# Performance work log

Measured on AMD Instinct MI355X. Metric: run time of the kernel, lower is better.

Reference implementation:

```python
import jax, jax.numpy as jnp
import numpy as np

N = 50000      # nodes
E = 600000     # edges
D = 128        # embedding_dim
H = 256        # GENConv MLP hidden = 2*D (expansion=2, num_layers=2)
L = 2          # n_layers
EPS_MSG = 1e-7
EPS_NORM = 1e-5


def setup_inputs() -> dict:
    key = jax.random.key(0)
    ks = jax.random.split(key, 16)
    s = 0.05
    inp = {}
    inp["x"] = jax.random.normal(ks[0], (N, 1), jnp.float32)
    inp["edge_index"] = jax.random.randint(ks[1], (2, E), 0, N)
    inp["edge_attr"] = jax.random.normal(ks[2], (E, 1), jnp.float32)
    # encoders
    inp["Wn"] = jax.random.normal(ks[3], (1, D), jnp.float32) * s
    inp["bn_b"] = jnp.zeros((D,), jnp.float32)
    inp["We"] = jax.random.normal(ks[4], (1, D), jnp.float32) * s
    inp["be"] = jnp.zeros((D,), jnp.float32)
    # per-layer BatchNorm affine
    inp["bn_gamma"] = jnp.ones((L, D), jnp.float32)
    inp["bn_beta"] = jnp.zeros((L, D), jnp.float32)
    # per-layer GENConv params: learnable temperature t, MLP [D->H->D] with LayerNorm
    inp["t"] = jnp.ones((L,), jnp.float32)
    inp["W1"] = jax.random.normal(ks[5], (L, D, H), jnp.float32) * s
    inp["b1"] = jnp.zeros((L, H), jnp.float32)
    inp["ln_g"] = jnp.ones((L, H), jnp.float32)
    inp["ln_b"] = jnp.zeros((L, H), jnp.float32)
    inp["W2"] = jax.random.normal(ks[6], (L, H, D), jnp.float32) * s
    inp["b2"] = jnp.zeros((L, D), jnp.float32)
    return inp


def _segment_softmax(logits, seg, num):
    # per-channel softmax over edges grouped by destination node
    m = jax.ops.segment_max(logits, seg, num_segments=num)
    m = jnp.where(jnp.isfinite(m), m, 0.0)  # empty segments
    ex = jnp.exp(logits - m[seg])
    den = jax.ops.segment_sum(ex, seg, num_segments=num)
    return ex / (den[seg] + 1e-16)


def reference(x, edge_index, edge_attr, Wn, bn_b, We, be,
              bn_gamma, bn_beta, t, W1, b1, ln_g, ln_b, W2, b2):
    src, dst = edge_index[0], edge_index[1]
    h = x @ Wn + bn_b                 # [N, D] node encoder
    e = edge_attr @ We + be           # [E, D] edge encoder
    for l in range(L):
        # DeepGCNLayer 'res+': h_in -> BN -> ReLU -> conv -> + h_in
        mu = h.mean(axis=0)
        var = h.var(axis=0)
        hn = (h - mu) / jnp.sqrt(var + EPS_NORM) * bn_gamma[l] + bn_beta[l]
        hn = jax.nn.relu(hn)
        # GENConv: msg = relu(x_j + e) + eps; softmax-aggr with temperature t
        msg = jax.nn.relu(hn[src] + e) + EPS_MSG          # [E, D]
        alpha = _segment_softmax(msg * t[l], dst, N)      # [E, D]
        agg = jax.ops.segment_sum(msg * alpha, dst, num_segments=N)  # [N, D]
        out = agg + hn                                    # add root
        # GENConv MLP: Linear -> LayerNorm -> ReLU -> Linear
        z = out @ W1[l] + b1[l]
        zm = z.mean(axis=-1, keepdims=True)
        zv = z.var(axis=-1, keepdims=True)
        z = (z - zm) / jnp.sqrt(zv + EPS_NORM) * ln_g[l] + ln_b[l]
        z = jax.nn.relu(z)
        z = z @ W2[l] + b2[l]
        h = h + z                                         # res+ residual
    # DotProductPredictor over the same edge list
    return (h[src] * h[dst]).sum(axis=-1)                 # [E]
```

## Files before the change

kernel.cpp:

```cpp
#include <hip/hip_runtime.h>
#include <hip/hip_bf16.h>
#include <math.h>

#define NN 50000
#define NE 600000
#define MPAD 50048
#define NS32 (MPAD / 32)
#define DIM 128
#define HID 256
#define NB 49
#define HIST_BLOCKS ((NE + 255) / 256)
#define CAST_BLOCKS ((4 * DIM * HID) / 256)
#define EPS_MSG 1e-7f
#define EPS_NORM 1e-5f

typedef __attribute__((ext_vector_type(8))) short short8v;
typedef __attribute__((ext_vector_type(8))) unsigned short ushort8v;
typedef __attribute__((ext_vector_type(4))) float f32x4;

__device__ inline ushort f2bf(float f) {
    union { float f; unsigned u; } v; v.f = f;
    unsigned r = v.u + 0x7FFF + ((v.u >> 16) & 1);
    return (ushort)(r >> 16);
}
__device__ inline float bf2f(ushort u) {
    union { unsigned u; float f; } v; v.u = (unsigned)u << 16; return v.f;
}

__global__ __launch_bounds__(256) void k_setup(const float* __restrict__ x,
                                               const int* __restrict__ dst,
                                               const float* __restrict__ W1,
                                               const float* __restrict__ W2,
                                               float* __restrict__ xs,
                                               int* __restrict__ deg,
                                               ushort* __restrict__ W1t,
                                               ushort* __restrict__ W2t) {
    int b = blockIdx.x;
    if (b < 64) {
        int lane = threadIdx.x & 63;
        float s = 0.f, q = 0.f;
        for (int i = b * 256 + threadIdx.x; i < NN; i += 64 * 256) {
            float v = x[i];
            s += v; q += v * v;
        }
        #pragma unroll
        for (int off = 32; off >= 1; off >>= 1) {
            s += __shfl_xor(s, off, 64);
            q += __shfl_xor(q, off, 64);
        }
        if (lane == 0) { atomicAdd(&xs[0], s); atomicAdd(&xs[1], q); }
    } else if (b < 64 + HIST_BLOCKS) {
        int i = (b - 64) * 256 + threadIdx.x;
        if (i < NE) atomicAdd(&deg[dst[i]], 1);
    } else {
        const int chunk = DIM * HID;
        int i = (b - 64 - HIST_BLOCKS) * 256 + threadIdx.x;
        int w = i / chunk;
        int j = i - w * chunk;
        if (w < 2) {
            int r = j / HID, c = j - r * HID;
            W1t[(size_t)w * chunk + (size_t)c * DIM + r] = f2bf(W1[(size_t)w * chunk + j]);
        } else {
            int l = w - 2;
            int r = j / DIM, c = j - r * DIM;
            W2t[(size_t)l * chunk + (size_t)c * HID + r] = f2bf(W2[(size_t)l * chunk + j]);
        }
    }
}

__global__ void k_hn0(const float* __restrict__ x, const float* __restrict__ xs,
                      const float* __restrict__ Wn, const float* __restrict__ bnb,
                      const float* __restrict__ gamma, const float* __restrict__ beta,
                      ushort* __restrict__ hn, int total4) {
    int i = blockIdx.x * blockDim.x + threadIdx.x;
    if (i >= total4) return;
    int d4 = (i & 31) * 4;
    int n = i >> 5;
    float mx = xs[0] * (1.f / NN);
    float vx = xs[1] * (1.f / NN) - mx * mx;
    float xv = x[n];
    float4 w = *(const float4*)(Wn + d4);
    float4 b = *(const float4*)(bnb + d4);
    float4 g = *(const float4*)(gamma + d4);
    float4 bt = *(const float4*)(beta + d4);
    ushort4 o;
    {
        float mu = fmaf(mx, w.x, b.x), sc = rsqrtf(vx * w.x * w.x + EPS_NORM) * g.x;
        o.x = f2bf(fmaxf(fmaf(fmaf(xv, w.x, b.x) - mu, sc, bt.x), 0.f));
    }
    {
        float mu = fmaf(mx, w.y, b.y), sc = rsqrtf(vx * w.y * w.y + EPS_NORM) * g.y;
        o.y = f2bf(fmaxf(fmaf(fmaf(xv, w.y, b.y) - mu, sc, bt.y), 0.f));
    }
    {
        float mu = fmaf(mx, w.z, b.z), sc = rsqrtf(vx * w.z * w.z + EPS_NORM) * g.z;
        o.z = f2bf(fmaxf(fmaf(fmaf(xv, w.z, b.z) - mu, sc, bt.z), 0.f));
    }
    {
        float mu = fmaf(mx, w.w, b.w), sc = rsqrtf(vx * w.w * w.w + EPS_NORM) * g.w;
        o.w = f2bf(fmaxf(fmaf(fmaf(xv, w.w, b.w) - mu, sc, bt.w), 0.f));
    }
    *(ushort4*)(hn + (size_t)n * DIM + d4) = o;
}

__global__ __launch_bounds__(256) void k_scanA(const int* __restrict__ deg,
                                               int* __restrict__ partials, int n) {
    __shared__ int ws[4];
    int b = blockIdx.x;
    int t = threadIdx.x;
    int s = 0;
    #pragma unroll
    for (int i = 0; i < 4; ++i) {
        int idx = b * 1024 + t + i * 256;
        s += (idx < n) ? deg[idx] : 0;
    }
    #pragma unroll
    for (int off = 32; off >= 1; off >>= 1) s += __shfl_xor(s, off, 64);
    if ((t & 63) == 0) ws[t >> 6] = s;
    __syncthreads();
    if (t == 0) partials[b] = ws[0] + ws[1] + ws[2] + ws[3];
}

__global__ __launch_bounds__(64) void k_scanB(const int* __restrict__ partials,
                                              int* __restrict__ base,
                                              int* __restrict__ row_off) {
    int t = threadIdx.x;
    int v = (t < NB) ? partials[t] : 0;
    int x = v;
    #pragma unroll
    for (int off = 1; off < 64; off <<= 1) {
        int y = __shfl_up(x, off, 64);
        if (t >= off) x += y;
    }
    if (t < NB) base[t] = x - v;
    if (t == 0) row_off[NN] = NE;
}

__global__ __launch_bounds__(1024) void k_scanC(const int* __restrict__ deg,
                                                const int* __restrict__ base,
                                                int* __restrict__ row_off,
                                                int* __restrict__ cursor, int n) {
    __shared__ int wsum[16];
    int i = blockIdx.x * 1024 + threadIdx.x;
    int lane = threadIdx.x & 63;
    int wid = threadIdx.x >> 6;
    int v = (i < n) ? deg[i] : 0;
    int x = v;
    #pragma unroll
    for (int off = 1; off < 64; off <<= 1) {
        int y = __shfl_up(x, off, 64);
        if (lane >= off) x += y;
    }
    if (lane == 63) wsum[wid] = x;
    __syncthreads();
    if (wid == 0 && lane < 16) {
        int w = wsum[lane];
        #pragma unroll
        for (int off = 1; off < 16; off <<= 1) {
            int y = __shfl_up(w, off, 64);
            if (lane >= off) w += y;
        }
        wsum[lane] = w;
    }
    __syncthreads();
    int prev = (wid == 0) ? 0 : wsum[wid - 1];
    int excl = base[blockIdx.x] + prev + (x - v);
    if (i < n) { row_off[i] = excl; cursor[i] = excl; }
}

__global__ void k_scatter(const int* __restrict__ src, const int* __restrict__ dst,
                          const float* __restrict__ eattr, int* __restrict__ cursor,
                          unsigned long long* __restrict__ erec, int E) {
    int i = blockIdx.x * blockDim.x + threadIdx.x;
    if (i >= E) return;
    int d = dst[i];
    int pos = atomicAdd(&cursor[d], 1);
    unsigned long long r = (unsigned long long)(unsigned)src[i]
                         | ((unsigned long long)(unsigned)i << 16)
                         | ((unsigned long long)f2bf(eattr[i]) << 36);
    erec[pos] = r;
}

__global__ __launch_bounds__(256) void k_bn_stats(const float* __restrict__ h,
                                                  float* __restrict__ stats) {
    __shared__ float red[2][128];
    int d = threadIdx.x & 127;
    int rsub = threadIdx.x >> 7;
    float s = 0.f, q = 0.f;
    for (int r = blockIdx.x * 2 + rsub; r < NN; r += gridDim.x * 2) {
        float v = h[(size_t)r * DIM + d];
        s += v; q += v * v;
    }
    if (rsub == 0) { red[0][d] = s; red[1][d] = q; }
    __syncthreads();
    if (rsub == 1) {
        atomicAdd(&stats[d], s + red[0][d]);
        atomicAdd(&stats[DIM + d], q + red[1][d]);
    }
}

__global__ void k_bn_relu(const float* __restrict__ h, const float* __restrict__ stats,
                          const float* __restrict__ gamma, const float* __restrict__ beta,
                          ushort* __restrict__ hn, int total4) {
    int i = blockIdx.x * blockDim.x + threadIdx.x;
    if (i >= total4) return;
    int d4 = (i & 31) * 4;
    int n = i >> 5;
    float4 v = *(const float4*)(h + (size_t)n * DIM + d4);
    float4 s = *(const float4*)(stats + d4);
    float4 q = *(const float4*)(stats + DIM + d4);
    float4 g = *(const float4*)(gamma + d4);
    float4 bt = *(const float4*)(beta + d4);
    ushort4 o;
    {
        float mu = s.x * (1.f / NN), var = q.x * (1.f / NN) - mu * mu;
        float sc = rsqrtf(var + EPS_NORM) * g.x;
        o.x = f2bf(fmaxf(fmaf(v.x - mu, sc, bt.x), 0.f));
    }
    {
        float mu = s.y * (1.f / NN), var = q.y * (1.f / NN) - mu * mu;
        float sc = rsqrtf(var + EPS_NORM) * g.y;
        o.y = f2bf(fmaxf(fmaf(v.y - mu, sc, bt.y), 0.f));
    }
    {
        float mu = s.z * (1.f / NN), var = q.z * (1.f / NN) - mu * mu;
        float sc = rsqrtf(var + EPS_NORM) * g.z;
        o.z = f2bf(fmaxf(fmaf(v.z - mu, sc, bt.z), 0.f));
    }
    {
        float mu = s.w * (1.f / NN), var = q.w * (1.f / NN) - mu * mu;
        float sc = rsqrtf(var + EPS_NORM) * g.w;
        o.w = f2bf(fmaxf(fmaf(v.w - mu, sc, bt.w), 0.f));
    }
    *(ushort4*)(hn + (size_t)n * DIM + d4) = o;
}

__global__ __launch_bounds__(256) void k_agg(const ushort* __restrict__ hn,
                                             const unsigned long long* __restrict__ erec,
                                             const int* __restrict__ row_off,
                                             const float* __restrict__ We,
                                             const float* __restrict__ be,
                                             const float* __restrict__ t_all, int l,
                                             ushort* __restrict__ ob, int N) {
    int n = blockIdx.x * 4 + (threadIdx.x >> 6);
    if (n >= N) return;
    int lane = threadIdx.x & 63;
    int d0 = lane * 2;
    float2 we = *(const float2*)(We + d0);
    float2 bd = *(const float2*)(be + d0);
    float t = t_all[l];
    int p0 = row_off[n], p1 = row_off[n + 1];
    int deg = p1 - p0;

    int mp = p0 + lane;
    unsigned long long r_l = (mp < p1) ? erec[mp] : 0ull;

    float den0 = 0.f, num0 = 0.f, den1 = 0.f, num1 = 0.f;
    int kmax = deg < 64 ? deg : 64;
    int k = 0;
    for (; k + 8 <= kmax; k += 8) {
        int ss[8]; float ee[8]; uint hv[8];
        #pragma unroll
        for (int u = 0; u < 8; ++u) {
            unsigned long long r = __shfl(r_l, k + u, 64);
            ss[u] = (int)(r & 0xFFFF);
            ee[u] = bf2f((ushort)(r >> 36));
        }
        #pragma unroll
        for (int u = 0; u < 8; ++u)
            hv[u] = *(const uint*)(hn + (size_t)ss[u] * DIM + d0);
        #pragma unroll
        for (int u = 0; u < 8; ++u) {
            float m0 = fmaxf(bf2f((ushort)hv[u]) + fmaf(ee[u], we.x, bd.x), 0.f) + EPS_MSG;
            float m1 = fmaxf(bf2f((ushort)(hv[u] >> 16)) + fmaf(ee[u], we.y, bd.y), 0.f) + EPS_MSG;
            float x0 = __expf(m0 * t), x1 = __expf(m1 * t);
            den0 += x0; num0 += m0 * x0; den1 += x1; num1 += m1 * x1;
        }
    }
    for (; k < kmax; ++k) {
        unsigned long long r = __shfl(r_l, k, 64);
        int s = (int)(r & 0xFFFF);
        float ea = bf2f((ushort)(r >> 36));
        uint hv = *(const uint*)(hn + (size_t)s * DIM + d0);
        float m0 = fmaxf(bf2f((ushort)hv) + fmaf(ea, we.x, bd.x), 0.f) + EPS_MSG;
        float m1 = fmaxf(bf2f((ushort)(hv >> 16)) + fmaf(ea, we.y, bd.y), 0.f) + EPS_MSG;
        float x0 = __expf(m0 * t), x1 = __expf(m1 * t);
        den0 += x0; num0 += m0 * x0; den1 += x1; num1 += m1 * x1;
    }
    for (int p = p0 + 64; p < p1; ++p) {
        unsigned long long r = erec[p];
        int s = (int)(r & 0xFFFF);
        float ea = bf2f((ushort)(r >> 36));
        uint hv = *(const uint*)(hn + (size_t)s * DIM + d0);
        float m0 = fmaxf(bf2f((ushort)hv) + fmaf(ea, we.x, bd.x), 0.f) + EPS_MSG;
        float m1 = fmaxf(bf2f((ushort)(hv >> 16)) + fmaf(ea, we.y, bd.y), 0.f) + EPS_MSG;
        float x0 = __expf(m0 * t), x1 = __expf(m1 * t);
        den0 += x0; num0 += m0 * x0; den1 += x1; num1 += m1 * x1;
    }
    uint hr = *(const uint*)(hn + (size_t)n * DIM + d0);
    float a0 = (deg > 0) ? num0 / (den0 + 1e-16f) : 0.f;
    float a1 = (deg > 0) ? num1 / (den1 + 1e-16f) : 0.f;
    uint o = (uint)f2bf(a0 + bf2f((ushort)hr)) |
             ((uint)f2bf(a1 + bf2f((ushort)(hr >> 16))) << 16);
    *(uint*)(ob + (size_t)n * DIM + d0) = o;
}

template <int FIRST>
__global__ __launch_bounds__(256, 1) void k_mlpw(const ushort* __restrict__ A,
                                                 const ushort* __restrict__ B1t,
                                                 const float* __restrict__ b1,
                                                 const float* __restrict__ g,
                                                 const float* __restrict__ bv,
                                                 const ushort* __restrict__ B2t,
                                                 const float* __restrict__ b2,
                                                 const float* __restrict__ x,
                                                 const float* __restrict__ Wn,
                                                 const float* __restrict__ bnb,
                                                 const float* __restrict__ Cin,
                                                 float* __restrict__ Cout,
                                                 ushort* __restrict__ hb,
                                                 ushort* Z) {
    constexpr int LW1 = 130;
    constexpr int LW2 = 258;
    __shared__ ushort W1s[256 * LW1];
    __shared__ ushort W2s[128 * LW2];
    const int tid = threadIdx.x;
    const int lane = tid & 63;
    const int wid = tid >> 6;
    const int l15 = lane & 15;
    const int lq = lane >> 4;

    #pragma unroll
    for (int i = 0; i < 16; ++i) {
        int e = (tid + i * 256) * 8;
        int r = e >> 7, c = e & 127;
        *(short8v*)(W1s + r * LW1 + c) = *(const short8v*)(B1t + r * 128 + c);
    }
    #pragma unroll
    for (int i = 0; i < 16; ++i) {
        int e = (tid + i * 256) * 8;
        int r = e >> 8, c = e & 255;
        *(short8v*)(W2s + r * LW2 + c) = *(const short8v*)(B2t + r * 256 + c);
    }
    float bb[16], gg[16], lb[16];
    #pragma unroll
    for (int nf = 0; nf < 16; ++nf) {
        int col = nf * 16 + l15;
        bb[nf] = b1[col]; gg[nf] = g[col]; lb[nf] = bv[col];
    }
    float b2v[8], wnc[8], bnc[8];
    #pragma unroll
    for (int nf = 0; nf < 8; ++nf) {
        int col = nf * 16 + l15;
        b2v[nf] = b2[col];
        wnc[nf] = FIRST ? Wn[col] : 0.f;
        bnc[nf] = FIRST ? bnb[col] : 0.f;
    }
    __syncthreads();

    for (int s = blockIdx.x * 4 + wid; s < NS32; s += 1024) {
        const int row0 = s * 32;
        short8v afr[4][2];
        #pragma unroll
        for (int ks = 0; ks < 4; ++ks)
            #pragma unroll
            for (int mi = 0; mi < 2; ++mi)
                afr[ks][mi] = *(const short8v*)(A + (size_t)(row0 + mi * 16 + l15) * DIM +
                                                ks * 32 + lq * 8);
        f32x4 acc[16][2] = {};
        #pragma unroll
        for (int ks = 0; ks < 4; ++ks) {
            int kk = ks * 32 + lq * 8;
            #pragma unroll
            for (int nf = 0; nf < 16; ++nf) {
                short8v bfr = *(const short8v*)(W1s + (nf * 16 + l15) * LW1 + kk);
                #pragma unroll
                for (int mi = 0; mi < 2; ++mi)
                    acc[nf][mi] = __builtin_amdgcn_mfma_f32_16x16x32_bf16(
                        afr[ks][mi], bfr, acc[nf][mi], 0, 0, 0);
            }
        }
        #pragma unroll
        for (int mi = 0; mi < 2; ++mi) {
            #pragma unroll
            for (int j = 0; j < 4; ++j) {
                float sum = 0.f, sq = 0.f;
                #pragma unroll
                for (int nf = 0; nf < 16; ++nf) {
                    float v = acc[nf][mi][j] + bb[nf];
                    acc[nf][mi][j] = v;
                    sum += v; sq += v * v;
                }
                #pragma unroll
                for (int off = 1; off <= 8; off <<= 1) {
                    sum += __shfl_xor(sum, off, 64);
                    sq += __shfl_xor(sq, off, 64);
                }
                float mu = sum * (1.f / HID);
                float var = sq * (1.f / HID) - mu * mu;
                float rs = rsqrtf(var + EPS_NORM);
                size_t rbase = (size_t)(row0 + mi * 16 + lq * 4 + j) * HID;
                #pragma unroll
                for (int nf = 0; nf < 16; ++nf) {
                    float v = fmaxf(fmaf((acc[nf][mi][j] - mu) * rs, gg[nf], lb[nf]), 0.f);
                    Z[rbase + nf * 16 + l15] = f2bf(v);
                }
            }
        }
        asm volatile("s_waitcnt vmcnt(0)" ::: "memory");
        short8v af2[2][8];
        #pragma unroll
        for (int mi = 0; mi < 2; ++mi)
            #pragma unroll
            for (int ks = 0; ks < 8; ++ks)
                af2[mi][ks] = *(const short8v*)(Z + (size_t)(row0 + mi * 16 + l15) * HID +
                                                ks * 32 + lq * 8);
        f32x4 acc2[8][2] = {};
        #pragma unroll
        for (int ks = 0; ks < 8; ++ks) {
            int kk = ks * 32 + lq * 8;
            #pragma unroll
            for (int nf = 0; nf < 8; ++nf) {
                short8v bf2 = *(const short8v*)(W2s + (nf * 16 + l15) * LW2 + kk);
                #pragma unroll
                for (int mi = 0; mi < 2; ++mi)
                    acc2[nf][mi] = __builtin_amdgcn_mfma_f32_16x16x32_bf16(
                        af2[mi][ks], bf2, acc2[nf][mi], 0, 0, 0);
            }
        }
        #pragma unroll
        for (int mi = 0; mi < 2; ++mi) {
            #pragma unroll
            for (int j = 0; j < 4; ++j) {
                int gr = row0 + mi * 16 + lq * 4 + j;
                float xb = 0.f;
                if (FIRST) xb = (gr < NN) ? x[gr] : 0.f;
                size_t rbase = (size_t)gr * DIM;
                #pragma unroll
                for (int nf = 0; nf < 8; ++nf) {
                    int col = nf * 16 + l15;
                    float base = FIRST ? fmaf(xb, wnc[nf], bnc[nf]) : Cin[rbase + col];
                    float v = acc2[nf][mi][j] + b2v[nf] + base;
                    if (FIRST) Cout[rbase + col] = v;
                    else hb[rbase + col] = f2bf(v);
                }
            }
        }
    }
}

__global__ __launch_bounds__(256) void k_dot(const ushort* __restrict__ hb,
                                             const unsigned long long* __restrict__ erec,
                                             const int* __restrict__ row_off,
                                             float* __restrict__ out, int N) {
    int n = blockIdx.x * 4 + (threadIdx.x >> 6);
    if (n >= N) return;
    int lane = threadIdx.x & 63;
    int sub = lane >> 4;
    int l16 = lane & 15;
    float hd[8];
    {
        ushort8v hv = *(const ushort8v*)(hb + (size_t)n * DIM + l16 * 8);
        #pragma unroll
        for (int j = 0; j < 8; ++j) hd[j] = bf2f(hv[j]);
    }
    int p0 = row_off[n], p1 = row_off[n + 1];
    int deg = p1 - p0;
    int mp = p0 + lane;
    unsigned long long r_l = (mp < p1) ? erec[mp] : 0ull;
    int kmax = deg < 64 ? deg : 64;
    for (int k = 0; k < kmax; k += 4) {
        int idx = k + sub;
        bool ok = idx < kmax;
        unsigned long long r = __shfl(r_l, idx, 64);
        int s = (int)(r & 0xFFFF);
        int e = (int)((r >> 16) & 0xFFFFF);
        ushort8v av = *(const ushort8v*)(hb + (size_t)(ok ? s : n) * DIM + l16 * 8);
        float p = 0.f;
        #pragma unroll
        for (int j = 0; j < 8; ++j) p = fmaf(bf2f(av[j]), hd[j], p);
        p += __shfl_xor(p, 1, 16);
        p += __shfl_xor(p, 2, 16);
        p += __shfl_xor(p, 4, 16);
        p += __shfl_xor(p, 8, 16);
        if (ok && l16 == 0) out[e] = p;
    }
    for (int pb = p0 + 64; pb < p1; pb += 4) {
        int pe = pb + sub;
        bool ok = pe < p1;
        int s = n, e = 0;
        if (ok) {
            unsigned long long r = erec[pe];
            s = (int)(r & 0xFFFF);
            e = (int)((r >> 16) & 0xFFFFF);
        }
        ushort8v av = *(const ushort8v*)(hb + (size_t)s * DIM + l16 * 8);
        float p = 0.f;
        #pragma unroll
        for (int j = 0; j < 8; ++j) p = fmaf(bf2f(av[j]), hd[j], p);
        p += __shfl_xor(p, 1, 16);
        p += __shfl_xor(p, 2, 16);
        p += __shfl_xor(p, 4, 16);
        p += __shfl_xor(p, 8, 16);
        if (ok && l16 == 0) out[e] = p;
    }
}

extern "C" void kernel_launch(void* const* d_in, const int* in_sizes, int n_in,
                              void* d_out, int out_size, void* d_ws, size_t ws_size,
                              hipStream_t stream) {
    const float* x        = (const float*)d_in[0];
    const int*   ei       = (const int*)d_in[1];
    const float* eattr    = (const float*)d_in[2];
    const float* Wn       = (const float*)d_in[3];
    const float* bnb      = (const float*)d_in[4];
    const float* We       = (const float*)d_in[5];
    const float* be       = (const float*)d_in[6];
    const float* bn_gamma = (const float*)d_in[7];
    const float* bn_beta  = (const float*)d_in[8];
    const float* t_all    = (const float*)d_in[9];
    const float* W1       = (const float*)d_in[10];
    const float* b1       = (const float*)d_in[11];
    const float* ln_g     = (const float*)d_in[12];
    const float* ln_b     = (const float*)d_in[13];
    const float* W2       = (const float*)d_in[14];
    const float* b2       = (const float*)d_in[15];
    float* out = (float*)d_out;

    const int N = NN, E = NE, D = DIM, H = HID;
    const int* src = ei;
    const int* dst = ei + E;

    char* ws = (char*)d_ws;
    auto alloc = [&](size_t bytes) {
        char* p = ws;
        ws += (bytes + 255) & ~(size_t)255;
        return p;
    };
    float*  h       = (float*)alloc((size_t)MPAD * D * 4);
    ushort* z       = (ushort*)alloc((size_t)MPAD * H * 2);
    ushort* ob      = (ushort*)alloc((size_t)MPAD * D * 2);
    ushort* hn      = (ushort*)alloc((size_t)MPAD * D * 2);
    ushort* hb      = (ushort*)alloc((size_t)MPAD * D * 2);
    ushort* W1t     = (ushort*)alloc((size_t)2 * D * H * 2);
    ushort* W2t     = (ushort*)alloc((size_t)2 * D * H * 2);
    unsigned long long* erec = (unsigned long long*)alloc((size_t)E * 8);
    int*    row_off = (int*)alloc((size_t)(N + 1) * 4);
    int*    cursor  = (int*)alloc((size_t)N * 4);
    int*    deg     = (int*)alloc((size_t)N * 4);
    int*    partials= (int*)alloc((size_t)64 * 4);
    int*    pbase   = (int*)alloc((size_t)64 * 4);
    float*  stats   = (float*)alloc((size_t)2 * D * 4);
    float*  xs      = (float*)alloc((size_t)2 * 4);

    hipMemsetAsync(deg, 0, (size_t)N * 4, stream);
    hipMemsetAsync(stats, 0, 1024 + 8, stream);

    k_setup<<<64 + HIST_BLOCKS + CAST_BLOCKS, 256, 0, stream>>>(x, dst, W1, W2,
                                                                xs, deg, W1t, W2t);
    k_scanA<<<NB, 256, 0, stream>>>(deg, partials, N);
    k_scanB<<<1, 64, 0, stream>>>(partials, pbase, row_off);
    k_scanC<<<NB, 1024, 0, stream>>>(deg, pbase, row_off, cursor, N);
    k_scatter<<<(E + 255) / 256, 256, 0, stream>>>(src, dst, eattr, cursor, erec, E);
    k_hn0<<<(N * 32 + 255) / 256, 256, 0, stream>>>(x, xs, Wn, bnb, bn_gamma, bn_beta,
                                                    hn, N * 32);

    k_agg<<<(N + 3) / 4, 256, 0, stream>>>(hn, erec, row_off, We, be, t_all, 0, ob, N);
    k_mlpw<1><<<256, 256, 0, stream>>>(ob, W1t, b1, ln_g, ln_b, W2t, b2,
                                       x, Wn, bnb, h, h, hb, z);
    k_bn_stats<<<256, 256, 0, stream>>>(h, stats);
    k_bn_relu<<<(N * 32 + 255) / 256, 256, 0, stream>>>(h, stats, bn_gamma + D, bn_beta + D,
                                                        hn, N * 32);

    k_agg<<<(N + 3) / 4, 256, 0, stream>>>(hn, erec, row_off, We, be, t_all, 1, ob, N);
    k_mlpw<0><<<256, 256, 0, stream>>>(ob, W1t + (size_t)D * H, b1 + H,
                                       ln_g + H, ln_b + H, W2t + (size_t)D * H, b2 + D,
                                       x, Wn, bnb, h, h, hb, z);

    k_dot<<<(N + 3) / 4, 256, 0, stream>>>(hb, erec, row_off, out, N);
}
```

Measured before the change: 396.4 us.

## Fuse BN statistics into MLP kernel, keep Z in LDS, store h as bf16

The first-layer MLP kernel now accumulates per-channel BatchNorm sums and squared sums in registers and adds them atomically, so the separate k_bn_stats pass is removed. The hidden activation Z stays in a per-wave XOR-swizzled LDS tile instead of a round trip through global memory. The fp32 h buffer is replaced by bf16 hb. Blocks drop to 3 waves, each handling 16-row tiles, to fit the extra LDS. Keeping the residual stream in bf16 lowers precision, and the MLP blocks have fewer waves to hide latency.

```diff
diff --git a/kernel.cpp b/kernel.cpp
--- a/kernel.cpp
+++ b/kernel.cpp
@@ -5,7 +5,7 @@
 #define NN 50000
 #define NE 600000
 #define MPAD 50048
-#define NS32 (MPAD / 32)
+#define NHS (MPAD / 16)
 #define DIM 128
 #define HID 256
 #define NB 49
@@ -13,6 +13,8 @@
 #define CAST_BLOCKS ((4 * DIM * HID) / 256)
 #define EPS_MSG 1e-7f
 #define EPS_NORM 1e-5f
+#define MLPW_WAVES 3
+#define MLPW_THREADS (MLPW_WAVES * 64)
 
 typedef __attribute__((ext_vector_type(8))) short short8v;
 typedef __attribute__((ext_vector_type(8))) unsigned short ushort8v;
@@ -181,32 +183,14 @@
     erec[pos] = r;
 }
 
-__global__ __launch_bounds__(256) void k_bn_stats(const float* __restrict__ h,
-                                                  float* __restrict__ stats) {
-    __shared__ float red[2][128];
-    int d = threadIdx.x & 127;
-    int rsub = threadIdx.x >> 7;
-    float s = 0.f, q = 0.f;
-    for (int r = blockIdx.x * 2 + rsub; r < NN; r += gridDim.x * 2) {
-        float v = h[(size_t)r * DIM + d];
-        s += v; q += v * v;
-    }
-    if (rsub == 0) { red[0][d] = s; red[1][d] = q; }
-    __syncthreads();
-    if (rsub == 1) {
-        atomicAdd(&stats[d], s + red[0][d]);
-        atomicAdd(&stats[DIM + d], q + red[1][d]);
-    }
-}
-
-__global__ void k_bn_relu(const float* __restrict__ h, const float* __restrict__ stats,
+__global__ void k_bn_relu(const ushort* __restrict__ hb, const float* __restrict__ stats,
                           const float* __restrict__ gamma, const float* __restrict__ beta,
                           ushort* __restrict__ hn, int total4) {
     int i = blockIdx.x * blockDim.x + threadIdx.x;
     if (i >= total4) return;
     int d4 = (i & 31) * 4;
     int n = i >> 5;
-    float4 v = *(const float4*)(h + (size_t)n * DIM + d4);
+    ushort4 hv = *(const ushort4*)(hb + (size_t)n * DIM + d4);
     float4 s = *(const float4*)(stats + d4);
     float4 q = *(const float4*)(stats + DIM + d4);
     float4 g = *(const float4*)(gamma + d4);
@@ -215,22 +199,22 @@
     {
         float mu = s.x * (1.f / NN), var = q.x * (1.f / NN) - mu * mu;
         float sc = rsqrtf(var + EPS_NORM) * g.x;
-        o.x = f2bf(fmaxf(fmaf(v.x - mu, sc, bt.x), 0.f));
+        o.x = f2bf(fmaxf(fmaf(bf2f(hv.x) - mu, sc, bt.x), 0.f));
     }
     {
         float mu = s.y * (1.f / NN), var = q.y * (1.f / NN) - mu * mu;
         float sc = rsqrtf(var + EPS_NORM) * g.y;
-        o.y = f2bf(fmaxf(fmaf(v.y - mu, sc, bt.y), 0.f));
+        o.y = f2bf(fmaxf(fmaf(bf2f(hv.y) - mu, sc, bt.y), 0.f));
     }
     {
         float mu = s.z * (1.f / NN), var = q.z * (1.f / NN) - mu * mu;
         float sc = rsqrtf(var + EPS_NORM) * g.z;
-        o.z = f2bf(fmaxf(fmaf(v.z - mu, sc, bt.z), 0.f));
+        o.z = f2bf(fmaxf(fmaf(bf2f(hv.z) - mu, sc, bt.z), 0.f));
     }
     {
         float mu = s.w * (1.f / NN), var = q.w * (1.f / NN) - mu * mu;
         float sc = rsqrtf(var + EPS_NORM) * g.w;
-        o.w = f2bf(fmaxf(fmaf(v.w - mu, sc, bt.w), 0.f));
+        o.w = f2bf(fmaxf(fmaf(bf2f(hv.w) - mu, sc, bt.w), 0.f));
     }
     *(ushort4*)(hn + (size_t)n * DIM + d4) = o;
 }
@@ -306,41 +290,42 @@
 }
 
 template <int FIRST>
-__global__ __launch_bounds__(256, 1) void k_mlpw(const ushort* __restrict__ A,
-                                                 const ushort* __restrict__ B1t,
-                                                 const float* __restrict__ b1,
-                                                 const float* __restrict__ g,
-                                                 const float* __restrict__ bv,
-                                                 const ushort* __restrict__ B2t,
-                                                 const float* __restrict__ b2,
-                                                 const float* __restrict__ x,
-                                                 const float* __restrict__ Wn,
-                                                 const float* __restrict__ bnb,
-                                                 const float* __restrict__ Cin,
-                                                 float* __restrict__ Cout,
-                                                 ushort* __restrict__ hb,
-                                                 ushort* Z) {
-    constexpr int LW1 = 130;
-    constexpr int LW2 = 258;
-    __shared__ ushort W1s[256 * LW1];
-    __shared__ ushort W2s[128 * LW2];
+__global__ __launch_bounds__(MLPW_THREADS, 1) void k_mlpw(const ushort* __restrict__ A,
+                                                          const ushort* __restrict__ B1t,
+                                                          const float* __restrict__ b1,
+                                                          const float* __restrict__ g,
+                                                          const float* __restrict__ bv,
+                                                          const ushort* __restrict__ B2t,
+                                                          const float* __restrict__ b2,
+                                                          const float* __restrict__ x,
+                                                          const float* __restrict__ Wn,
+                                                          const float* __restrict__ bnb,
+                                                          const ushort* hbin,
+                                                          ushort* hbout,
+                                                          float* __restrict__ stats) {
+    __shared__ ushort W1s[256 * 128];
+    __shared__ ushort W2s[128 * 256];
+    __shared__ ushort Zs[MLPW_WAVES][16 * 256];
     const int tid = threadIdx.x;
     const int lane = tid & 63;
     const int wid = tid >> 6;
     const int l15 = lane & 15;
     const int lq = lane >> 4;
-
-    #pragma unroll
-    for (int i = 0; i < 16; ++i) {
-        int e = (tid + i * 256) * 8;
-        int r = e >> 7, c = e & 127;
-        *(short8v*)(W1s + r * LW1 + c) = *(const short8v*)(B1t + r * 128 + c);
-    }
-    #pragma unroll
-    for (int i = 0; i < 16; ++i) {
-        int e = (tid + i * 256) * 8;
-        int r = e >> 8, c = e & 255;
-        *(short8v*)(W2s + r * LW2 + c) = *(const short8v*)(B2t + r * 256 + c);
+    char* const w1b = (char*)W1s;
+    char* const w2b = (char*)W2s;
+    char* const zb = (char*)Zs[wid];
+
+    for (int c = tid; c < 4096; c += MLPW_THREADS) {
+        int r = c >> 4;
+        int cb = (c & 15) * 16;
+        *(short8v*)(w1b + r * 256 + (cb ^ ((r & 15) << 4))) =
+            *(const short8v*)(B1t + r * 128 + cb / 2);
+    }
+    for (int c = tid; c < 4096; c += MLPW_THREADS) {
+        int r = c >> 5;
+        int cb = (c & 31) * 16;
+        *(short8v*)(w2b + r * 512 + (cb ^ ((r & 15) << 4))) =
+            *(const short8v*)(B2t + r * 256 + cb / 2);
     }
     float bb[16], gg[16], lb[16];
     #pragma unroll
@@ -356,94 +341,96 @@
         wnc[nf] = FIRST ? Wn[col] : 0.f;
         bnc[nf] = FIRST ? bnb[col] : 0.f;
     }
+    float ss[8] = {}, sqv[8] = {};
     __syncthreads();
 
-    for (int s = blockIdx.x * 4 + wid; s < NS32; s += 1024) {
-        const int row0 = s * 32;
-        short8v afr[4][2];
+    for (int hs = blockIdx.x * MLPW_WAVES + wid; hs < NHS; hs += 256 * MLPW_WAVES) {
+        const int row0 = hs * 16;
+        short8v afr[4];
         #pragma unroll
         for (int ks = 0; ks < 4; ++ks)
-            #pragma unroll
-            for (int mi = 0; mi < 2; ++mi)
-                afr[ks][mi] = *(const short8v*)(A + (size_t)(row0 + mi * 16 + l15) * DIM +
-                                                ks * 32 + lq * 8);
-        f32x4 acc[16][2] = {};
+            afr[ks] = *(const short8v*)(A + (size_t)(row0 + l15) * DIM + ks * 32 + lq * 8);
+        f32x4 acc[16] = {};
         #pragma unroll
         for (int ks = 0; ks < 4; ++ks) {
-            int kk = ks * 32 + lq * 8;
+            int cb = (ks * 64 + lq * 16) ^ (l15 << 4);
             #pragma unroll
             for (int nf = 0; nf < 16; ++nf) {
-                short8v bfr = *(const short8v*)(W1s + (nf * 16 + l15) * LW1 + kk);
-                #pragma unroll
-                for (int mi = 0; mi < 2; ++mi)
-                    acc[nf][mi] = __builtin_amdgcn_mfma_f32_16x16x32_bf16(
-                        afr[ks][mi], bfr, acc[nf][mi], 0, 0, 0);
-            }
-        }
-        #pragma unroll
-        for (int mi = 0; mi < 2; ++mi) {
+                short8v bfr = *(const short8v*)(w1b + (nf * 16 + l15) * 256 + cb);
+                acc[nf] = __builtin_amdgcn_mfma_f32_16x16x32_bf16(afr[ks], bfr, acc[nf],
+                                                                  0, 0, 0);
+            }
+        }
+        #pragma unroll
+        for (int j = 0; j < 4; ++j) {
+            float sum = 0.f, sq = 0.f;
             #pragma unroll
-            for (int j = 0; j < 4; ++j) {
-                float sum = 0.f, sq = 0.f;
-                #pragma unroll
-                for (int nf = 0; nf < 16; ++nf) {
-                    float v = acc[nf][mi][j] + bb[nf];
-                    acc[nf][mi][j] = v;
-                    sum += v; sq += v * v;
-                }
-                #pragma unroll
-                for (int off = 1; off <= 8; off <<= 1) {
-                    sum += __shfl_xor(sum, off, 64);
-                    sq += __shfl_xor(sq, off, 64);
-                }
-                float mu = sum * (1.f / HID);
-                float var = sq * (1.f / HID) - mu * mu;
-                float rs = rsqrtf(var + EPS_NORM);
-                size_t rbase = (size_t)(row0 + mi * 16 + lq * 4 + j) * HID;
-                #pragma unroll
-                for (int nf = 0; nf < 16; ++nf) {
-                    float v = fmaxf(fmaf((acc[nf][mi][j] - mu) * rs, gg[nf], lb[nf]), 0.f);
-                    Z[rbase + nf * 16 + l15] = f2bf(v);
-                }
-            }
-        }
-        asm volatile("s_waitcnt vmcnt(0)" ::: "memory");
-        short8v af2[2][8];
-        #pragma unroll
-        for (int mi = 0; mi < 2; ++mi)
+            for (int nf = 0; nf < 16; ++nf) {
+                float v = acc[nf][j] + bb[nf];
+                acc[nf][j] = v;
+                sum += v; sq += v * v;
+            }
             #pragma unroll
-            for (int ks = 0; ks < 8; ++ks)
-                af2[mi][ks] = *(const short8v*)(Z + (size_t)(row0 + mi * 16 + l15) * HID +
-                                                ks * 32 + lq * 8);
-        f32x4 acc2[8][2] = {};
+            for (int off = 1; off <= 8; off <<= 1) {
+                sum += __shfl_xor(sum, off, 64);
+                sq += __shfl_xor(sq, off, 64);
+            }
+            float mu = sum * (1.f / HID);
+            float var = sq * (1.f / HID) - mu * mu;
+            float rs = rsqrtf(var + EPS_NORM);
+            int row = lq * 4 + j;
+            #pragma unroll
+            for (int nf = 0; nf < 16; ++nf) {
+                float v = fmaxf(fmaf((acc[nf][j] - mu) * rs, gg[nf], lb[nf]), 0.f);
+                int cbz = ((nf * 16 + l15) * 2) ^ ((row & 15) << 4);
+                *(ushort*)(zb + row * 512 + cbz) = f2bf(v);
+            }
+        }
+        short8v az[8];
+        #pragma unroll
+        for (int ks = 0; ks < 8; ++ks)
+            az[ks] = *(const short8v*)(zb + l15 * 512 + ((ks * 64 + lq * 16) ^ (l15 << 4)));
+        f32x4 acc2[8] = {};
         #pragma unroll
         for (int ks = 0; ks < 8; ++ks) {
-            int kk = ks * 32 + lq * 8;
+            int cb = (ks * 64 + lq * 16) ^ (l15 << 4);
             #pragma unroll
             for (int nf = 0; nf < 8; ++nf) {
-                short8v bf2 = *(const short8v*)(W2s + (nf * 16 + l15) * LW2 + kk);
-                #pragma unroll
-                for (int mi = 0; mi < 2; ++mi)
-                    acc2[nf][mi] = __builtin_amdgcn_mfma_f32_16x16x32_bf16(
-                        af2[mi][ks], bf2, acc2[nf][mi], 0, 0, 0);
-            }
-        }
-        #pragma unroll
-        for (int mi = 0; mi < 2; ++mi) {
+                short8v bfr = *(const short8v*)(w2b + (nf * 16 + l15) * 512 + cb);
+                acc2[nf] = __builtin_amdgcn_mfma_f32_16x16x32_bf16(az[ks], bfr, acc2[nf],
+                                                                   0, 0, 0);
+            }
+        }
+        #pragma unroll
+        for (int j = 0; j < 4; ++j) {
+            int gr = row0 + lq * 4 + j;
+            float xb = 0.f;
+            if (FIRST) xb = (gr < NN) ? x[gr] : 0.f;
+            size_t rbase = (size_t)gr * DIM;
+            bool ok = gr < NN;
             #pragma unroll
-            for (int j = 0; j < 4; ++j) {
-                int gr = row0 + mi * 16 + lq * 4 + j;
-                float xb = 0.f;
-                if (FIRST) xb = (gr < NN) ? x[gr] : 0.f;
-                size_t rbase = (size_t)gr * DIM;
-                #pragma unroll
-                for (int nf = 0; nf < 8; ++nf) {
-                    int col = nf * 16 + l15;
-                    float base = FIRST ? fmaf(xb, wnc[nf], bnc[nf]) : Cin[rbase + col];
-                    float v = acc2[nf][mi][j] + b2v[nf] + base;
-                    if (FIRST) Cout[rbase + col] = v;
-                    else hb[rbase + col] = f2bf(v);
+            for (int nf = 0; nf < 8; ++nf) {
+                int col = nf * 16 + l15;
+                float base = FIRST ? fmaf(xb, wnc[nf], bnc[nf]) : bf2f(hbin[rbase + col]);
+                float v = acc2[nf][j] + b2v[nf] + base;
+                hbout[rbase + col] = f2bf(v);
+                if (FIRST) {
+                    ss[nf] += ok ? v : 0.f;
+                    sqv[nf] += ok ? v * v : 0.f;
                 }
+            }
+        }
+    }
+    if (FIRST) {
+        #pragma unroll
+        for (int nf = 0; nf < 8; ++nf) {
+            float s = ss[nf], q = sqv[nf];
+            s += __shfl_xor(s, 16, 64); s += __shfl_xor(s, 32, 64);
+            q += __shfl_xor(q, 16, 64); q += __shfl_xor(q, 32, 64);
+            if (lq == 0) {
+                int col = nf * 16 + l15;
+                atomicAdd(&stats[col], s);
+                atomicAdd(&stats[DIM + col], q);
             }
         }
     }
@@ -537,8 +524,6 @@
         ws += (bytes + 255) & ~(size_t)255;
         return p;
     };
-    float*  h       = (float*)alloc((size_t)MPAD * D * 4);
-    ushort* z       = (ushort*)alloc((size_t)MPAD * H * 2);
     ushort* ob      = (ushort*)alloc((size_t)MPAD * D * 2);
     ushort* hn      = (ushort*)alloc((size_t)MPAD * D * 2);
     ushort* hb      = (ushort*)alloc((size_t)MPAD * D * 2);
@@ -566,16 +551,15 @@
                                                     hn, N * 32);
 
     k_agg<<<(N + 3) / 4, 256, 0, stream>>>(hn, erec, row_off, We, be, t_all, 0, ob, N);
-    k_mlpw<1><<<256, 256, 0, stream>>>(ob, W1t, b1, ln_g, ln_b, W2t, b2,
-                                       x, Wn, bnb, h, h, hb, z);
-    k_bn_stats<<<256, 256, 0, stream>>>(h, stats);
-    k_bn_relu<<<(N * 32 + 255) / 256, 256, 0, stream>>>(h, stats, bn_gamma + D, bn_beta + D,
-                                                        hn, N * 32);
+    k_mlpw<1><<<256, MLPW_THREADS, 0, stream>>>(ob, W1t, b1, ln_g, ln_b, W2t, b2,
+                                                x, Wn, bnb, hb, hb, stats);
+    k_bn_relu<<<(N * 32 + 255) / 256, 256, 0, stream>>>(hb, stats, bn_gamma + D,
+                                                        bn_beta + D, hn, N * 32);
 
     k_agg<<<(N + 3) / 4, 256, 0, stream>>>(hn, erec, row_off, We, be, t_all, 1, ob, N);
-    k_mlpw<0><<<256, 256, 0, stream>>>(ob, W1t + (size_t)D * H, b1 + H,
-                                       ln_g + H, ln_b + H, W2t + (size_t)D * H, b2 + D,
-                                       x, Wn, bnb, h, h, hb, z);
+    k_mlpw<0><<<256, MLPW_THREADS, 0, stream>>>(ob, W1t + (size_t)D * H, b1 + H,
+                                                ln_g + H, ln_b + H, W2t + (size_t)D * H,
+                                                b2 + D, x, Wn, bnb, hb, hb, stats);
 
     k_dot<<<(N + 3) / 4, 256, 0, stream>>>(hb, erec, row_off, out, N);
 }
```

Result: slower. 431.4 us (+8.8%).
